# Kernel tuning notes

Measured on AMD Instinct MI355X. Metric: run time of the kernel, lower is better.

## Reference

```python
import jax, jax.numpy as jnp
import numpy as np
import math

B, S, D, H = 2, 2048, 4096, 32
HD = D // H          # 128 head dim
HALF = HD // 2       # 64 rotary pairs
AL = 10              # adapter length


def setup_inputs() -> dict:
    key = jax.random.key(0)
    ks = jax.random.split(key, 8)
    sc = 0.02
    x = jax.random.normal(ks[0], (B, S, D), jnp.float32)
    adapter = jax.random.normal(ks[1], (B, AL, D), jnp.float32)
    wq = jax.random.normal(ks[2], (D, D), jnp.float32) * sc
    wk = jax.random.normal(ks[3], (D, D), jnp.float32) * sc
    wv = jax.random.normal(ks[4], (D, D), jnp.float32) * sc
    wo = jax.random.normal(ks[5], (D, D), jnp.float32) * sc
    gate = jax.random.normal(ks[6], (1, H, 1, 1), jnp.float32) * 0.1
    # rotary frequencies (LLaMA convention), freqs_cis = exp(i * t * f)
    inv_freq = 1.0 / (10000.0 ** (np.arange(0, HD, 2).astype(np.float32) / HD))
    ang = np.outer(np.arange(S, dtype=np.float32), inv_freq)  # [S, HALF]
    cos = jnp.asarray(np.cos(ang), jnp.float32)
    sin = jnp.asarray(np.sin(ang), jnp.float32)
    # additive causal mask [1,1,S,S]
    mask = jnp.triu(jnp.full((S, S), -1e9, jnp.float32), 1)[None, None]
    return {"x": x, "mask": mask, "cos": cos, "sin": sin, "wq": wq,
            "wk": wk, "wv": wv, "wo": wo, "gate": gate,
            "adapter": adapter, "start_pos": 0}


def _rope(t, cos, sin):
    # t: [B,S,H,HD]; complex rotate consecutive pairs
    tr = t.reshape(*t.shape[:-1], HALF, 2)
    t0, t1 = tr[..., 0], tr[..., 1]
    c = cos[None, :, None, :]  # [1,S,1,HALF]
    s = sin[None, :, None, :]
    r0 = t0 * c - t1 * s
    r1 = t0 * s + t1 * c
    return jnp.stack([r0, r1], axis=-1).reshape(t.shape)


def reference(x, mask, cos, sin, wq, wk, wv, wo, gate, adapter, start_pos):
    bsz, seqlen, _ = x.shape
    scale = 1.0 / math.sqrt(HD)
    xq = (x @ wq.T).reshape(bsz, seqlen, H, HD)
    xk = (x @ wk.T).reshape(bsz, seqlen, H, HD)
    xv = (x @ wv.T).reshape(bsz, seqlen, H, HD)
    xq = _rope(xq, cos, sin)
    xk = _rope(xk, cos, sin)
    # training path: keys/values = current tokens (start_pos == 0)
    q = xq.transpose(0, 2, 1, 3)   # [B,H,S,HD]
    k = xk.transpose(0, 2, 1, 3)
    v = xv.transpose(0, 2, 1, 3)
    scores = jnp.einsum('bhqd,bhkd->bhqk', q, k) * scale + mask
    scores = jax.nn.softmax(scores.astype(jnp.float32), axis=-1).astype(x.dtype)
    out = jnp.einsum('bhqk,bhkd->bhqd', scores, v)
    # gated adapter cross-attention (adapter_len > 1 branch)
    a_len = adapter.shape[1]
    a_v = (adapter @ wv.T).reshape(bsz, a_len, H, HD).transpose(0, 2, 1, 3)
    a_k = (adapter @ wk.T).reshape(bsz, a_len, H, HD).transpose(0, 2, 1, 3)
    a_scores = jnp.einsum('bhqd,bhkd->bhqk', q, a_k) * scale
    a_scores = jnp.tanh(gate) * jax.nn.softmax(
        a_scores.astype(jnp.float32), axis=-1).astype(x.dtype)
    out = out + jnp.einsum('bhqk,bhkd->bhqd', a_scores, a_v)
    out = out.transpose(0, 2, 1, 3).reshape(bsz, seqlen, -1)
    return out @ wo.T
```

## Files before the change

kernel.cpp:

```cpp
#include <hip/hip_runtime.h>
#include <hip/hip_bf16.h>
#include <stdint.h>

#define B_ 2
#define S_ 2048
#define D_ 4096
#define H_ 32
#define HD_ 128
#define HALF_ 64
#define AL_ 10
#define MROWS (B_*S_)

typedef __hip_bfloat16 bf16;
typedef __attribute__((ext_vector_type(8))) __bf16 bf16x8;
typedef __attribute__((ext_vector_type(4))) float f32x4;
typedef __attribute__((ext_vector_type(4))) unsigned short us4;

__device__ __forceinline__ void gld_lds16(const void* g, void* l) {
    __builtin_amdgcn_global_load_lds((const __attribute__((address_space(1))) void*)g,
                                     (__attribute__((address_space(3))) void*)l, 16, 0, 0);
}

__global__ void detect_dtype(const unsigned short* __restrict__ x, int* __restrict__ flag) {
    __shared__ int cnt;
    if (threadIdx.x == 0) cnt = 0;
    __syncthreads();
    int bad = 0;
#pragma unroll
    for (int i = 0; i < 16; i++) {
        unsigned int u = x[threadIdx.x * 16 + i];
        float v = __uint_as_float(u << 16);
        if (!(fabsf(v) < 1000.f)) bad++;
    }
    atomicAdd(&cnt, bad);
    __syncthreads();
    if (threadIdx.x == 0) flag[0] = (cnt > 64) ? 1 : 0;
}

__global__ void convert_bf16(const void* __restrict__ in, bf16* __restrict__ out,
                             const int* __restrict__ flag, int n) {
    int i = (blockIdx.x * 256 + threadIdx.x) * 4;
    if (i >= n) return;
    if (flag[0]) {
        float4 f = *(const float4*)((const float*)in + i);
        out[i + 0] = __float2bfloat16(f.x);
        out[i + 1] = __float2bfloat16(f.y);
        out[i + 2] = __float2bfloat16(f.z);
        out[i + 3] = __float2bfloat16(f.w);
    } else {
        *(us4*)(out + i) = *(const us4*)((const unsigned short*)in + i);
    }
}

template<int MODE>
__global__ __launch_bounds__(256) void gemm_bt(
    const bf16* __restrict__ A, const bf16* __restrict__ W,
    const bf16* __restrict__ cosb, const bf16* __restrict__ sinb,
    void* __restrict__ outv, const int* __restrict__ flag, int K)
{
    __shared__ __align__(16) bf16 sA[128*64];
    __shared__ __align__(16) bf16 sB[128*64];
    const int tid  = threadIdx.x;
    const int wave = tid >> 6, lane = tid & 63;
    const int quad = lane >> 4, col = lane & 15;
    const int m0 = blockIdx.y * 128, n0 = blockIdx.x * 128;
    const int wm = (wave >> 1) * 64, wn = (wave & 1) * 64;

    bool f32o = false;
    if (MODE == 2) f32o = (flag[0] != 0);

    f32x4 acc[4][4];
#pragma unroll
    for (int i = 0; i < 4; i++)
#pragma unroll
        for (int j = 0; j < 4; j++) acc[i][j] = {0.f, 0.f, 0.f, 0.f};

    for (int k0 = 0; k0 < K; k0 += 64) {
        __syncthreads();
#pragma unroll
        for (int i = 0; i < 4; i++) {
            int c   = i * 256 + tid;
            int row = c >> 3;
            int cc  = (c & 7) ^ (row & 7);
            gld_lds16(A + (size_t)(m0 + row) * K + k0 + cc * 8,
                      sA + (size_t)(i * 256 + wave * 64) * 8);
            gld_lds16(W + (size_t)(n0 + row) * K + k0 + cc * 8,
                      sB + (size_t)(i * 256 + wave * 64) * 8);
        }
        __syncthreads();

#pragma unroll
        for (int kk = 0; kk < 64; kk += 32) {
            bf16x8 af[4], bfr[4];
#pragma unroll
            for (int mt = 0; mt < 4; mt++) {
                int r  = wm + mt * 16 + col;
                int ck = ((kk >> 3) + quad) ^ (r & 7);
                af[mt] = *(const bf16x8*)(sA + r * 64 + ck * 8);
            }
#pragma unroll
            for (int nt = 0; nt < 4; nt++) {
                int r  = wn + nt * 16 + col;
                int ck = ((kk >> 3) + quad) ^ (r & 7);
                bfr[nt] = *(const bf16x8*)(sB + r * 64 + ck * 8);
            }
#pragma unroll
            for (int mt = 0; mt < 4; mt++)
#pragma unroll
                for (int nt = 0; nt < 4; nt++)
                    acc[mt][nt] = __builtin_amdgcn_mfma_f32_16x16x32_bf16(
                        af[mt], bfr[nt], acc[mt][nt], 0, 0, 0);
        }
    }

#pragma unroll
    for (int mt = 0; mt < 4; mt++) {
#pragma unroll
        for (int nt = 0; nt < 4; nt++) {
            int n = n0 + wn + nt * 16 + col;
#pragma unroll
            for (int e = 0; e < 4; e++) {
                int m   = m0 + wm + mt * 16 + quad * 4 + e;
                float v = acc[mt][nt][e];
                if (MODE == 2) {
                    if (f32o) ((float*)outv)[(size_t)m * D_ + n] = v;
                    else      ((bf16*)outv)[(size_t)m * D_ + n] = __float2bfloat16(v);
                } else {
                    int b = m >> 11, s = m & (S_ - 1);
                    int h = n >> 7,  hd = n & (HD_ - 1);
                    bf16* out = (bf16*)outv;
                    if (MODE == 0) {
                        float other = __shfl_xor(v, 1);
                        float c  = __bfloat162float(cosb[s * HALF_ + (hd >> 1)]);
                        float sn = __bfloat162float(sinb[s * HALF_ + (hd >> 1)]);
                        float r  = (hd & 1) ? (v * c + other * sn)
                                            : (v * c - other * sn);
                        out[((size_t)(b * H_ + h) * S_ + s) * HD_ + hd] = __float2bfloat16(r);
                    } else {
                        out[((size_t)(b * H_ + h) * HD_ + hd) * S_ + s] = __float2bfloat16(v);
                    }
                }
            }
        }
    }
}

__global__ __launch_bounds__(256, 2) void attn_fwd(
    const bf16* __restrict__ q, const bf16* __restrict__ k,
    const bf16* __restrict__ vT, bf16* __restrict__ o)
{
    __shared__ __align__(16) bf16 smem[24576];
    bf16* sK = smem;
    bf16* sV = smem + 8192;
    bf16* sP = smem + 16384;

    const int tid  = threadIdx.x, wave = tid >> 6, lane = tid & 63;
    const int quad = lane >> 4, col = lane & 15;
    const int qt = (gridDim.x - 1) - blockIdx.x;
    const int bh = blockIdx.y;
    const int q0 = qt * 128;
    const bf16* qb = q  + (size_t)bh * S_ * HD_;
    const bf16* kb = k  + (size_t)bh * S_ * HD_;
    const bf16* vb = vT + (size_t)bh * HD_ * S_;

#pragma unroll
    for (int i = 0; i < 8; i++) {
        int c = i * 256 + tid;
        int row = c >> 4;
        int cc  = (c & 15) ^ (row & 7);
        gld_lds16(qb + (size_t)(q0 + row) * HD_ + cc * 8,
                  smem + (size_t)(i * 256 + wave * 64) * 8);
    }
    __syncthreads();

    bf16x8 qf[2][4];
#pragma unroll
    for (int rq = 0; rq < 2; rq++) {
        int row = wave * 32 + rq * 16 + col;
#pragma unroll
        for (int kkI = 0; kkI < 4; kkI++) {
            int ck = (kkI * 4 + quad) ^ (row & 7);
            qf[rq][kkI] = *(const bf16x8*)(smem + row * 128 + ck * 8);
        }
    }

    float mst[2][4], lst[2][4];
#pragma unroll
    for (int rq = 0; rq < 2; rq++)
#pragma unroll
        for (int e = 0; e < 4; e++) { mst[rq][e] = -1e30f; lst[rq][e] = 0.f; }
    f32x4 oacc[2][8];
#pragma unroll
    for (int rq = 0; rq < 2; rq++)
#pragma unroll
        for (int i = 0; i < 8; i++) oacc[rq][i] = {0.f, 0.f, 0.f, 0.f};

    const float scale = 0.08838834764831845f;
    const int ktEnd = 2 * qt + 2;

    for (int kt = 0; kt < ktEnd; kt++) {
        const int k0 = kt * 64;
        __syncthreads();
#pragma unroll
        for (int i = 0; i < 4; i++) {
            int c = i * 256 + tid;
            int rowK = c >> 4, ccK = (c & 15) ^ (rowK & 7);
            gld_lds16(kb + (size_t)(k0 + rowK) * HD_ + ccK * 8,
                      sK + (size_t)(i * 256 + wave * 64) * 8);
            int rowV = c >> 3, ccV = (c & 7) ^ (rowV & 7);
            gld_lds16(vb + (size_t)rowV * S_ + k0 + ccV * 8,
                      sV + (size_t)(i * 256 + wave * 64) * 8);
        }
        __syncthreads();

        f32x4 sc[2][4];
#pragma unroll
        for (int rq = 0; rq < 2; rq++)
#pragma unroll
            for (int nt = 0; nt < 4; nt++) sc[rq][nt] = {0.f, 0.f, 0.f, 0.f};
#pragma unroll
        for (int kkI = 0; kkI < 4; kkI++) {
#pragma unroll
            for (int nt = 0; nt < 4; nt++) {
                int rk  = nt * 16 + col;
                int ckk = (kkI * 4 + quad) ^ (rk & 7);
                bf16x8 bk = *(const bf16x8*)(sK + rk * 128 + ckk * 8);
                sc[0][nt] = __builtin_amdgcn_mfma_f32_16x16x32_bf16(qf[0][kkI], bk, sc[0][nt], 0, 0, 0);
                sc[1][nt] = __builtin_amdgcn_mfma_f32_16x16x32_bf16(qf[1][kkI], bk, sc[1][nt], 0, 0, 0);
            }
        }

        const bool diag = (kt >= 2 * qt);
#pragma unroll
        for (int rq = 0; rq < 2; rq++)
#pragma unroll
            for (int nt = 0; nt < 4; nt++)
#pragma unroll
                for (int e = 0; e < 4; e++) {
                    float v = sc[rq][nt][e] * scale;
                    if (diag && (k0 + nt * 16 + col > q0 + wave * 32 + rq * 16 + quad * 4 + e))
                        v = -1e30f;
                    sc[rq][nt][e] = v;
                }

        float alpha_[2][4];
#pragma unroll
        for (int rq = 0; rq < 2; rq++)
#pragma unroll
            for (int e = 0; e < 4; e++) {
                float mx = fmaxf(fmaxf(sc[rq][0][e], sc[rq][1][e]),
                                 fmaxf(sc[rq][2][e], sc[rq][3][e]));
#pragma unroll
                for (int off = 1; off < 16; off <<= 1) mx = fmaxf(mx, __shfl_xor(mx, off));
                float mnew = fmaxf(mst[rq][e], mx);
                float al   = __expf(mst[rq][e] - mnew);
                float rs   = 0.f;
                int prow = wave * 32 + rq * 16 + quad * 4 + e;
#pragma unroll
                for (int nt = 0; nt < 4; nt++) {
                    float p = __expf(sc[rq][nt][e] - mnew);
                    rs += p;
                    int pcol = nt * 16 + col;
                    int pc   = (pcol >> 3) ^ (prow & 7);
                    sP[prow * 64 + pc * 8 + (pcol & 7)] = __float2bfloat16(p);
                }
#pragma unroll
                for (int off = 1; off < 16; off <<= 1) rs += __shfl_xor(rs, off);
                lst[rq][e] = lst[rq][e] * al + rs;
                mst[rq][e] = mnew;
                alpha_[rq][e] = al;
            }
#pragma unroll
        for (int rq = 0; rq < 2; rq++)
#pragma unroll
            for (int nt = 0; nt < 8; nt++)
#pragma unroll
                for (int e = 0; e < 4; e++) oacc[rq][nt][e] *= alpha_[rq][e];

#pragma unroll
        for (int kkI = 0; kkI < 2; kkI++) {
            bf16x8 pf[2];
#pragma unroll
            for (int rq = 0; rq < 2; rq++) {
                int rp  = wave * 32 + rq * 16 + col;
                int ckp = (kkI * 4 + quad) ^ (rp & 7);
                pf[rq] = *(const bf16x8*)(sP + rp * 64 + ckp * 8);
            }
#pragma unroll
            for (int nt = 0; nt < 8; nt++) {
                int rv  = nt * 16 + col;
                int ckv = (kkI * 4 + quad) ^ (rv & 7);
                bf16x8 vf = *(const bf16x8*)(sV + rv * 64 + ckv * 8);
                oacc[0][nt] = __builtin_amdgcn_mfma_f32_16x16x32_bf16(pf[0], vf, oacc[0][nt], 0, 0, 0);
                oacc[1][nt] = __builtin_amdgcn_mfma_f32_16x16x32_bf16(pf[1], vf, oacc[1][nt], 0, 0, 0);
            }
        }
    }

    const int b = bh >> 5, h = bh & (H_ - 1);
#pragma unroll
    for (int rq = 0; rq < 2; rq++)
#pragma unroll
        for (int e = 0; e < 4; e++) {
            int s = q0 + wave * 32 + rq * 16 + quad * 4 + e;
            float inv = 1.f / lst[rq][e];
#pragma unroll
            for (int nt = 0; nt < 8; nt++) {
                int hd = nt * 16 + col;
                o[((size_t)(b * S_ + s) * H_ + h) * HD_ + hd] =
                    __float2bfloat16(oacc[rq][nt][e] * inv);
            }
        }
}

__global__ __launch_bounds__(256) void adapter_kv(
    const bf16* __restrict__ adp, const bf16* __restrict__ wk,
    const bf16* __restrict__ wv, float* __restrict__ ak, float* __restrict__ av)
{
    const int tid = threadIdx.x, wave = tid >> 6, lane = tid & 63;
    const int gid = blockIdx.x * 4 + wave;
    const int n = gid & (D_ - 1), b = gid >> 12;
    const bf16* w    = blockIdx.y ? wv : wk;
    float*      outp = blockIdx.y ? av : ak;

    float acc[AL_];
#pragma unroll
    for (int j = 0; j < AL_; j++) acc[j] = 0.f;

    for (int t = 0; t < 8; t++) {
        int kb = t * 512 + lane * 8;
        bf16x8 w8 = *(const bf16x8*)(w + (size_t)n * D_ + kb);
        float wf[8];
#pragma unroll
        for (int i = 0; i < 8; i++) wf[i] = (float)w8[i];
#pragma unroll
        for (int j = 0; j < AL_; j++) {
            bf16x8 a8 = *(const bf16x8*)(adp + (size_t)(b * AL_ + j) * D_ + kb);
            float s = 0.f;
#pragma unroll
            for (int i = 0; i < 8; i++) s += (float)a8[i] * wf[i];
            acc[j] += s;
        }
    }
#pragma unroll
    for (int j = 0; j < AL_; j++) {
        float v = acc[j];
#pragma unroll
        for (int off = 1; off < 64; off <<= 1) v += __shfl_xor(v, off);
        if (lane == 0) outp[(size_t)(b * AL_ + j) * D_ + n] = v;
    }
}

__global__ __launch_bounds__(256) void adapter_add(
    const bf16* __restrict__ q, const float* __restrict__ ak,
    const float* __restrict__ av, const bf16* __restrict__ gate,
    bf16* __restrict__ o)
{
    const int tid = threadIdx.x, wave = tid >> 6, lane = tid & 63;
    const int g = blockIdx.x * 4 + wave;
    const int s = g & (S_ - 1);
    const int h = (g >> 11) & (H_ - 1);
    const int b = g >> 16;
    const int hd = lane * 2;

    const bf16* qp = q + ((size_t)(b * H_ + h) * S_ + s) * HD_ + hd;
    float q0f = __bfloat162float(qp[0]);
    float q1f = __bfloat162float(qp[1]);
    const float scale = 0.08838834764831845f;

    float sc[AL_];
#pragma unroll
    for (int j = 0; j < AL_; j++) {
        const float* akp = ak + (size_t)(b * AL_ + j) * D_ + h * HD_ + hd;
        float p = q0f * akp[0] + q1f * akp[1];
#pragma unroll
        for (int off = 1; off < 64; off <<= 1) p += __shfl_xor(p, off);
        sc[j] = p * scale;
    }
    float mx = sc[0];
#pragma unroll
    for (int j = 1; j < AL_; j++) mx = fmaxf(mx, sc[j]);
    float sum = 0.f;
#pragma unroll
    for (int j = 0; j < AL_; j++) { sc[j] = __expf(sc[j] - mx); sum += sc[j]; }
    float wgt = tanhf(__bfloat162float(gate[h])) / sum;

    float a0 = 0.f, a1 = 0.f;
#pragma unroll
    for (int j = 0; j < AL_; j++) {
        const float* avp = av + (size_t)(b * AL_ + j) * D_ + h * HD_ + hd;
        a0 += sc[j] * avp[0];
        a1 += sc[j] * avp[1];
    }
    bf16* op = o + ((size_t)(b * S_ + s) * H_ + h) * HD_ + hd;
    op[0] = __float2bfloat16(__bfloat162float(op[0]) + wgt * a0);
    op[1] = __float2bfloat16(__bfloat162float(op[1]) + wgt * a1);
}

extern "C" void kernel_launch(void* const* d_in, const int* in_sizes, int n_in,
                              void* d_out, int out_size, void* d_ws, size_t ws_size,
                              hipStream_t stream)
{
    const void* x_raw    = d_in[0];
    const void* cos_raw  = d_in[2];
    const void* sin_raw  = d_in[3];
    const void* wq_raw   = d_in[4];
    const void* wk_raw   = d_in[5];
    const void* wv_raw   = d_in[6];
    const void* wo_raw   = d_in[7];
    const void* gate_raw = d_in[8];
    const void* adp_raw  = d_in[9];

    const size_t NE = (size_t)B_ * S_ * D_;
    const int    CS = S_ * HALF_;
    const int    AD = B_ * AL_ * D_;

    bf16* xc   = (bf16*)d_ws;
    bf16* wqc  = xc  + NE;
    bf16* wkc  = wqc + NE;
    bf16* wvc  = wkc + NE;
    bf16* woc  = wvc + NE;
    bf16* qb   = woc + NE;
    bf16* kb   = qb  + NE;
    bf16* vb   = kb  + NE;
    bf16* cosc = vb  + NE;
    bf16* sinc = cosc + CS;
    bf16* adpc = sinc + CS;
    bf16* gatec= adpc + AD;
    float* akb = (float*)(gatec + 32);
    float* avb = akb + AD;
    int*  flag = (int*)(avb + AD);
    bf16* ab   = xc;

    dim3 blk(256);
    detect_dtype<<<1, 256, 0, stream>>>((const unsigned short*)x_raw, flag);

    convert_bf16<<<dim3((int)(NE/4 + 255) / 256), blk, 0, stream>>>(x_raw,  xc,  flag, (int)NE);
    convert_bf16<<<dim3((int)(NE/4 + 255) / 256), blk, 0, stream>>>(wq_raw, wqc, flag, (int)NE);
    convert_bf16<<<dim3((int)(NE/4 + 255) / 256), blk, 0, stream>>>(wk_raw, wkc, flag, (int)NE);
    convert_bf16<<<dim3((int)(NE/4 + 255) / 256), blk, 0, stream>>>(wv_raw, wvc, flag, (int)NE);
    convert_bf16<<<dim3((int)(NE/4 + 255) / 256), blk, 0, stream>>>(wo_raw, woc, flag, (int)NE);
    convert_bf16<<<dim3((CS/4 + 255) / 256), blk, 0, stream>>>(cos_raw,  cosc, flag, CS);
    convert_bf16<<<dim3((CS/4 + 255) / 256), blk, 0, stream>>>(sin_raw,  sinc, flag, CS);
    convert_bf16<<<dim3((AD/4 + 255) / 256), blk, 0, stream>>>(adp_raw,  adpc, flag, AD);
    convert_bf16<<<dim3(1), blk, 0, stream>>>(gate_raw, gatec, flag, 32);

    dim3 gg(D_ / 128, MROWS / 128);
    gemm_bt<0><<<gg, blk, 0, stream>>>(xc, wqc, cosc, sinc, qb, flag, D_);
    gemm_bt<0><<<gg, blk, 0, stream>>>(xc, wkc, cosc, sinc, kb, flag, D_);
    gemm_bt<1><<<gg, blk, 0, stream>>>(xc, wvc, cosc, sinc, vb, flag, D_);
    adapter_kv<<<dim3(2048, 2), blk, 0, stream>>>(adpc, wkc, wvc, akb, avb);
    attn_fwd<<<dim3(S_ / 128, B_ * H_), blk, 0, stream>>>(qb, kb, vb, ab);
    adapter_add<<<dim3(B_ * H_ * S_ / 4), blk, 0, stream>>>(qb, akb, avb, gatec, ab);
    gemm_bt<2><<<gg, blk, 0, stream>>>(ab, woc, cosc, sinc, d_out, flag, D_);
}
```

Before: 1.480 ms.

## Double-buffer K/V in flash attention with 8 waves of 16 rows each

Restructures the attention kernel to use 512 threads (8 waves), each owning 16 query rows instead of 32, and loads Q fragments straight from global memory. K/V tiles are double-buffered in LDS, with the next tile prefetched via global_load_lds while the current one is computed, and raw s_waitcnt/s_barrier replace the two syncthreads per iteration. Waves skip fully masked causal tiles and raise their priority around the MFMA sections. This aims to hide K/V load latency and raise occupancy, at the cost of more LDS per block and hand-counted vmcnt waits that are fragile.

```diff
diff --git a/kernel.cpp b/kernel.cpp
--- a/kernel.cpp
+++ b/kernel.cpp
@@ -145,120 +145,118 @@
     }
 }
 
-__global__ __launch_bounds__(256, 2) void attn_fwd(
+__global__ __launch_bounds__(512, 4) void attn_fwd(
     const bf16* __restrict__ q, const bf16* __restrict__ k,
     const bf16* __restrict__ vT, bf16* __restrict__ o)
 {
-    __shared__ __align__(16) bf16 smem[24576];
-    bf16* sK = smem;
-    bf16* sV = smem + 8192;
-    bf16* sP = smem + 16384;
+    __shared__ __align__(16) bf16 smem[40960];
+    bf16* sP = smem + 32768;
 
     const int tid  = threadIdx.x, wave = tid >> 6, lane = tid & 63;
     const int quad = lane >> 4, col = lane & 15;
     const int qt = (gridDim.x - 1) - blockIdx.x;
     const int bh = blockIdx.y;
     const int q0 = qt * 128;
+    const int row0 = q0 + wave * 16;
+    const int rmax = row0 + 15;
     const bf16* qb = q  + (size_t)bh * S_ * HD_;
     const bf16* kb = k  + (size_t)bh * S_ * HD_;
     const bf16* vb = vT + (size_t)bh * HD_ * S_;
 
-#pragma unroll
-    for (int i = 0; i < 8; i++) {
-        int c = i * 256 + tid;
-        int row = c >> 4;
-        int cc  = (c & 15) ^ (row & 7);
-        gld_lds16(qb + (size_t)(q0 + row) * HD_ + cc * 8,
-                  smem + (size_t)(i * 256 + wave * 64) * 8);
-    }
-    __syncthreads();
-
-    bf16x8 qf[2][4];
-#pragma unroll
-    for (int rq = 0; rq < 2; rq++) {
-        int row = wave * 32 + rq * 16 + col;
-#pragma unroll
-        for (int kkI = 0; kkI < 4; kkI++) {
-            int ck = (kkI * 4 + quad) ^ (row & 7);
-            qf[rq][kkI] = *(const bf16x8*)(smem + row * 128 + ck * 8);
-        }
-    }
-
-    float mst[2][4], lst[2][4];
-#pragma unroll
-    for (int rq = 0; rq < 2; rq++)
-#pragma unroll
-        for (int e = 0; e < 4; e++) { mst[rq][e] = -1e30f; lst[rq][e] = 0.f; }
-    f32x4 oacc[2][8];
-#pragma unroll
-    for (int rq = 0; rq < 2; rq++)
-#pragma unroll
-        for (int i = 0; i < 8; i++) oacc[rq][i] = {0.f, 0.f, 0.f, 0.f};
+    bf16x8 qf[4];
+#pragma unroll
+    for (int kkI = 0; kkI < 4; kkI++)
+        qf[kkI] = *(const bf16x8*)(qb + (size_t)(row0 + col) * HD_ + (kkI * 4 + quad) * 8);
+
+    float mst[4], lst[4];
+#pragma unroll
+    for (int e = 0; e < 4; e++) { mst[e] = -1e30f; lst[e] = 0.f; }
+    f32x4 oacc[8];
+#pragma unroll
+    for (int i = 0; i < 8; i++) oacc[i] = {0.f, 0.f, 0.f, 0.f};
+
+#pragma unroll
+    for (int i = 0; i < 2; i++) {
+        int c = i * 512 + tid;
+        int rowK = c >> 4, ccK = (c & 15) ^ (rowK & 7);
+        gld_lds16(kb + (size_t)rowK * HD_ + ccK * 8,
+                  smem + (size_t)(i * 512 + wave * 64) * 8);
+        int rowV = c >> 3, ccV = (c & 7) ^ (rowV & 7);
+        gld_lds16(vb + (size_t)rowV * S_ + ccV * 8,
+                  smem + 16384 + (size_t)(i * 512 + wave * 64) * 8);
+    }
 
     const float scale = 0.08838834764831845f;
     const int ktEnd = 2 * qt + 2;
+    int cur = 0;
 
     for (int kt = 0; kt < ktEnd; kt++) {
         const int k0 = kt * 64;
-        __syncthreads();
-#pragma unroll
-        for (int i = 0; i < 4; i++) {
-            int c = i * 256 + tid;
-            int rowK = c >> 4, ccK = (c & 15) ^ (rowK & 7);
-            gld_lds16(kb + (size_t)(k0 + rowK) * HD_ + ccK * 8,
-                      sK + (size_t)(i * 256 + wave * 64) * 8);
-            int rowV = c >> 3, ccV = (c & 7) ^ (rowV & 7);
-            gld_lds16(vb + (size_t)rowV * S_ + k0 + ccV * 8,
-                      sV + (size_t)(i * 256 + wave * 64) * 8);
-        }
-        __syncthreads();
-
-        f32x4 sc[2][4];
-#pragma unroll
-        for (int rq = 0; rq < 2; rq++)
-#pragma unroll
-            for (int nt = 0; nt < 4; nt++) sc[rq][nt] = {0.f, 0.f, 0.f, 0.f};
-#pragma unroll
-        for (int kkI = 0; kkI < 4; kkI++) {
-#pragma unroll
-            for (int nt = 0; nt < 4; nt++) {
-                int rk  = nt * 16 + col;
-                int ckk = (kkI * 4 + quad) ^ (rk & 7);
-                bf16x8 bk = *(const bf16x8*)(sK + rk * 128 + ckk * 8);
-                sc[0][nt] = __builtin_amdgcn_mfma_f32_16x16x32_bf16(qf[0][kkI], bk, sc[0][nt], 0, 0, 0);
-                sc[1][nt] = __builtin_amdgcn_mfma_f32_16x16x32_bf16(qf[1][kkI], bk, sc[1][nt], 0, 0, 0);
-            }
-        }
-
-        const bool diag = (kt >= 2 * qt);
-#pragma unroll
-        for (int rq = 0; rq < 2; rq++)
+        bf16* sKc = smem + cur * 8192;
+        bf16* sVc = smem + 16384 + cur * 8192;
+
+        if (kt + 1 < ktEnd) {
+            const int kn = k0 + 64;
+            bf16* sKn = smem + (cur ^ 1) * 8192;
+            bf16* sVn = smem + 16384 + (cur ^ 1) * 8192;
+#pragma unroll
+            for (int i = 0; i < 2; i++) {
+                int c = i * 512 + tid;
+                int rowK = c >> 4, ccK = (c & 15) ^ (rowK & 7);
+                gld_lds16(kb + (size_t)(kn + rowK) * HD_ + ccK * 8,
+                          sKn + (size_t)(i * 512 + wave * 64) * 8);
+                int rowV = c >> 3, ccV = (c & 7) ^ (rowV & 7);
+                gld_lds16(vb + (size_t)rowV * S_ + kn + ccV * 8,
+                          sVn + (size_t)(i * 512 + wave * 64) * 8);
+            }
+            asm volatile("s_waitcnt vmcnt(4)" ::: "memory");
+        } else {
+            asm volatile("s_waitcnt vmcnt(0)" ::: "memory");
+        }
+        asm volatile("s_barrier" ::: "memory");
+
+        if (k0 <= rmax) {
+            f32x4 sc[4];
+#pragma unroll
+            for (int nt = 0; nt < 4; nt++) sc[nt] = {0.f, 0.f, 0.f, 0.f};
+            __builtin_amdgcn_s_setprio(1);
+#pragma unroll
+            for (int kkI = 0; kkI < 4; kkI++) {
+#pragma unroll
+                for (int nt = 0; nt < 4; nt++) {
+                    int rk  = nt * 16 + col;
+                    int ckk = (kkI * 4 + quad) ^ (rk & 7);
+                    bf16x8 bk = *(const bf16x8*)(sKc + rk * 128 + ckk * 8);
+                    sc[nt] = __builtin_amdgcn_mfma_f32_16x16x32_bf16(qf[kkI], bk, sc[nt], 0, 0, 0);
+                }
+            }
+            __builtin_amdgcn_s_setprio(0);
+
+            const bool diag = (k0 + 63 > row0);
 #pragma unroll
             for (int nt = 0; nt < 4; nt++)
 #pragma unroll
                 for (int e = 0; e < 4; e++) {
-                    float v = sc[rq][nt][e] * scale;
-                    if (diag && (k0 + nt * 16 + col > q0 + wave * 32 + rq * 16 + quad * 4 + e))
+                    float v = sc[nt][e] * scale;
+                    if (diag && (k0 + nt * 16 + col > row0 + quad * 4 + e))
                         v = -1e30f;
-                    sc[rq][nt][e] = v;
+                    sc[nt][e] = v;
                 }
 
-        float alpha_[2][4];
-#pragma unroll
-        for (int rq = 0; rq < 2; rq++)
+            float alpha_[4];
 #pragma unroll
             for (int e = 0; e < 4; e++) {
-                float mx = fmaxf(fmaxf(sc[rq][0][e], sc[rq][1][e]),
-                                 fmaxf(sc[rq][2][e], sc[rq][3][e]));
+                float mx = fmaxf(fmaxf(sc[0][e], sc[1][e]),
+                                 fmaxf(sc[2][e], sc[3][e]));
 #pragma unroll
                 for (int off = 1; off < 16; off <<= 1) mx = fmaxf(mx, __shfl_xor(mx, off));
-                float mnew = fmaxf(mst[rq][e], mx);
-                float al   = __expf(mst[rq][e] - mnew);
+                float mnew = fmaxf(mst[e], mx);
+                float al   = __expf(mst[e] - mnew);
                 float rs   = 0.f;
-                int prow = wave * 32 + rq * 16 + quad * 4 + e;
+                int prow = wave * 16 + quad * 4 + e;
 #pragma unroll
                 for (int nt = 0; nt < 4; nt++) {
-                    float p = __expf(sc[rq][nt][e] - mnew);
+                    float p = __expf(sc[nt][e] - mnew);
                     rs += p;
                     int pcol = nt * 16 + col;
                     int pc   = (pcol >> 3) ^ (prow & 7);
@@ -266,51 +264,48 @@
                 }
 #pragma unroll
                 for (int off = 1; off < 16; off <<= 1) rs += __shfl_xor(rs, off);
-                lst[rq][e] = lst[rq][e] * al + rs;
-                mst[rq][e] = mnew;
-                alpha_[rq][e] = al;
-            }
-#pragma unroll
-        for (int rq = 0; rq < 2; rq++)
+                lst[e] = lst[e] * al + rs;
+                mst[e] = mnew;
+                alpha_[e] = al;
+            }
 #pragma unroll
             for (int nt = 0; nt < 8; nt++)
 #pragma unroll
-                for (int e = 0; e < 4; e++) oacc[rq][nt][e] *= alpha_[rq][e];
-
-#pragma unroll
-        for (int kkI = 0; kkI < 2; kkI++) {
-            bf16x8 pf[2];
-#pragma unroll
-            for (int rq = 0; rq < 2; rq++) {
-                int rp  = wave * 32 + rq * 16 + col;
+                for (int e = 0; e < 4; e++) oacc[nt][e] *= alpha_[e];
+
+            __builtin_amdgcn_s_setprio(1);
+#pragma unroll
+            for (int kkI = 0; kkI < 2; kkI++) {
+                int rp  = wave * 16 + col;
                 int ckp = (kkI * 4 + quad) ^ (rp & 7);
-                pf[rq] = *(const bf16x8*)(sP + rp * 64 + ckp * 8);
-            }
-#pragma unroll
-            for (int nt = 0; nt < 8; nt++) {
-                int rv  = nt * 16 + col;
-                int ckv = (kkI * 4 + quad) ^ (rv & 7);
-                bf16x8 vf = *(const bf16x8*)(sV + rv * 64 + ckv * 8);
-                oacc[0][nt] = __builtin_amdgcn_mfma_f32_16x16x32_bf16(pf[0], vf, oacc[0][nt], 0, 0, 0);
-                oacc[1][nt] = __builtin_amdgcn_mfma_f32_16x16x32_bf16(pf[1], vf, oacc[1][nt], 0, 0, 0);
-            }
-        }
+                bf16x8 pf = *(const bf16x8*)(sP + rp * 64 + ckp * 8);
+#pragma unroll
+                for (int nt = 0; nt < 8; nt++) {
+                    int rv  = nt * 16 + col;
+                    int ckv = (kkI * 4 + quad) ^ (rv & 7);
+                    bf16x8 vf = *(const bf16x8*)(sVc + rv * 64 + ckv * 8);
+                    oacc[nt] = __builtin_amdgcn_mfma_f32_16x16x32_bf16(pf, vf, oacc[nt], 0, 0, 0);
+                }
+            }
+            __builtin_amdgcn_s_setprio(0);
+        }
+
+        asm volatile("s_barrier" ::: "memory");
+        cur ^= 1;
     }
 
     const int b = bh >> 5, h = bh & (H_ - 1);
 #pragma unroll
-    for (int rq = 0; rq < 2; rq++)
-#pragma unroll
-        for (int e = 0; e < 4; e++) {
-            int s = q0 + wave * 32 + rq * 16 + quad * 4 + e;
-            float inv = 1.f / lst[rq][e];
-#pragma unroll
-            for (int nt = 0; nt < 8; nt++) {
-                int hd = nt * 16 + col;
-                o[((size_t)(b * S_ + s) * H_ + h) * HD_ + hd] =
-                    __float2bfloat16(oacc[rq][nt][e] * inv);
-            }
-        }
+    for (int e = 0; e < 4; e++) {
+        int s = q0 + wave * 16 + quad * 4 + e;
+        float inv = 1.f / lst[e];
+#pragma unroll
+        for (int nt = 0; nt < 8; nt++) {
+            int hd = nt * 16 + col;
+            o[((size_t)(b * S_ + s) * H_ + h) * HD_ + hd] =
+                __float2bfloat16(oacc[nt][e] * inv);
+        }
+    }
 }
 
 __global__ __launch_bounds__(256) void adapter_kv(
@@ -450,7 +445,7 @@
     gemm_bt<0><<<gg, blk, 0, stream>>>(xc, wkc, cosc, sinc, kb, flag, D_);
     gemm_bt<1><<<gg, blk, 0, stream>>>(xc, wvc, cosc, sinc, vb, flag, D_);
     adapter_kv<<<dim3(2048, 2), blk, 0, stream>>>(adpc, wkc, wvc, akb, avb);
-    attn_fwd<<<dim3(S_ / 128, B_ * H_), blk, 0, stream>>>(qb, kb, vb, ab);
+    attn_fwd<<<dim3(S_ / 128, B_ * H_), dim3(512), 0, stream>>>(qb, kb, vb, ab);
     adapter_add<<<dim3(B_ * H_ * S_ / 4), blk, 0, stream>>>(qb, akb, avb, gatec, ab);
     gemm_bt<2><<<gg, blk, 0, stream>>>(ab, woc, cosc, sinc, d_out, flag, D_);
 }
```

After: 1.435 ms. -3.0%, faster.

## Double-buffer K/V in attention with 512-thread blocks and lazy softmax rescaling

Applied to the files above, without the earlier changes.

Rewrites the attention kernel to use 512-thread blocks covering 256 query rows, and double-buffers K/V tiles in LDS so the next tile's global loads overlap compute, using manual waitcnt and barriers. Q is loaded straight into registers. The softmax scale is folded into the Q projection epilogue. Exp is done via exp2, and the running max is only rescaled when the new max exceeds the old by more than a threshold. Waves skip fully masked tiles, MFMA sections get raised priority, and the P buffer uses an extra swizzle. The trade-off is more LDS per block and a lazy-rescale path that may lose precision in edge cases.

```diff
diff --git a/kernel.cpp b/kernel.cpp
--- a/kernel.cpp
+++ b/kernel.cpp
@@ -56,7 +56,7 @@
 __global__ __launch_bounds__(256) void gemm_bt(
     const bf16* __restrict__ A, const bf16* __restrict__ W,
     const bf16* __restrict__ cosb, const bf16* __restrict__ sinb,
-    void* __restrict__ outv, const int* __restrict__ flag, int K)
+    void* __restrict__ outv, const int* __restrict__ flag, int K, float oscale)
 {
     __shared__ __align__(16) bf16 sA[128*64];
     __shared__ __align__(16) bf16 sB[128*64];
@@ -135,7 +135,8 @@
                         float sn = __bfloat162float(sinb[s * HALF_ + (hd >> 1)]);
                         float r  = (hd & 1) ? (v * c + other * sn)
                                             : (v * c - other * sn);
-                        out[((size_t)(b * H_ + h) * S_ + s) * HD_ + hd] = __float2bfloat16(r);
+                        out[((size_t)(b * H_ + h) * S_ + s) * HD_ + hd] =
+                            __float2bfloat16(r * oscale);
                     } else {
                         out[((size_t)(b * H_ + h) * HD_ + hd) * S_ + s] = __float2bfloat16(v);
                     }
@@ -145,44 +146,31 @@
     }
 }
 
-__global__ __launch_bounds__(256, 2) void attn_fwd(
+__global__ __launch_bounds__(512, 2) void attn_fwd(
     const bf16* __restrict__ q, const bf16* __restrict__ k,
     const bf16* __restrict__ vT, bf16* __restrict__ o)
 {
-    __shared__ __align__(16) bf16 smem[24576];
-    bf16* sK = smem;
-    bf16* sV = smem + 8192;
-    bf16* sP = smem + 16384;
+    __shared__ __align__(16) bf16 smem[49152];
+    bf16* sP = smem + 32768;
 
     const int tid  = threadIdx.x, wave = tid >> 6, lane = tid & 63;
     const int quad = lane >> 4, col = lane & 15;
     const int qt = (gridDim.x - 1) - blockIdx.x;
     const int bh = blockIdx.y;
-    const int q0 = qt * 128;
+    const int q0 = qt * 256;
+    const int row0 = q0 + wave * 32;
+    const int rmax = row0 + 31;
     const bf16* qb = q  + (size_t)bh * S_ * HD_;
     const bf16* kb = k  + (size_t)bh * S_ * HD_;
     const bf16* vb = vT + (size_t)bh * HD_ * S_;
 
-#pragma unroll
-    for (int i = 0; i < 8; i++) {
-        int c = i * 256 + tid;
-        int row = c >> 4;
-        int cc  = (c & 15) ^ (row & 7);
-        gld_lds16(qb + (size_t)(q0 + row) * HD_ + cc * 8,
-                  smem + (size_t)(i * 256 + wave * 64) * 8);
-    }
-    __syncthreads();
-
     bf16x8 qf[2][4];
 #pragma unroll
-    for (int rq = 0; rq < 2; rq++) {
-        int row = wave * 32 + rq * 16 + col;
-#pragma unroll
-        for (int kkI = 0; kkI < 4; kkI++) {
-            int ck = (kkI * 4 + quad) ^ (row & 7);
-            qf[rq][kkI] = *(const bf16x8*)(smem + row * 128 + ck * 8);
-        }
-    }
+    for (int rq = 0; rq < 2; rq++)
+#pragma unroll
+        for (int kkI = 0; kkI < 4; kkI++)
+            qf[rq][kkI] = *(const bf16x8*)(qb + (size_t)(row0 + rq * 16 + col) * HD_
+                                              + (kkI * 4 + quad) * 8);
 
     float mst[2][4], lst[2][4];
 #pragma unroll
@@ -195,106 +183,174 @@
 #pragma unroll
         for (int i = 0; i < 8; i++) oacc[rq][i] = {0.f, 0.f, 0.f, 0.f};
 
-    const float scale = 0.08838834764831845f;
-    const int ktEnd = 2 * qt + 2;
+#pragma unroll
+    for (int i = 0; i < 2; i++) {
+        int c = i * 512 + tid;
+        int rowK = c >> 4, ccK = (c & 15) ^ (rowK & 7);
+        gld_lds16(kb + (size_t)rowK * HD_ + ccK * 8,
+                  smem + (size_t)(i * 512 + wave * 64) * 8);
+        int rowV = c >> 3, ccV = (c & 7) ^ (rowV & 7);
+        gld_lds16(vb + (size_t)rowV * S_ + ccV * 8,
+                  smem + 16384 + (size_t)(i * 512 + wave * 64) * 8);
+    }
+
+    const float L2E = 1.44269504088896f;
+    const int ktEnd = 4 * qt + 4;
+    int cur = 0;
 
     for (int kt = 0; kt < ktEnd; kt++) {
         const int k0 = kt * 64;
-        __syncthreads();
-#pragma unroll
-        for (int i = 0; i < 4; i++) {
-            int c = i * 256 + tid;
-            int rowK = c >> 4, ccK = (c & 15) ^ (rowK & 7);
-            gld_lds16(kb + (size_t)(k0 + rowK) * HD_ + ccK * 8,
-                      sK + (size_t)(i * 256 + wave * 64) * 8);
-            int rowV = c >> 3, ccV = (c & 7) ^ (rowV & 7);
-            gld_lds16(vb + (size_t)rowV * S_ + k0 + ccV * 8,
-                      sV + (size_t)(i * 256 + wave * 64) * 8);
-        }
-        __syncthreads();
-
-        f32x4 sc[2][4];
-#pragma unroll
-        for (int rq = 0; rq < 2; rq++)
-#pragma unroll
-            for (int nt = 0; nt < 4; nt++) sc[rq][nt] = {0.f, 0.f, 0.f, 0.f};
-#pragma unroll
-        for (int kkI = 0; kkI < 4; kkI++) {
-#pragma unroll
-            for (int nt = 0; nt < 4; nt++) {
-                int rk  = nt * 16 + col;
-                int ckk = (kkI * 4 + quad) ^ (rk & 7);
-                bf16x8 bk = *(const bf16x8*)(sK + rk * 128 + ckk * 8);
-                sc[0][nt] = __builtin_amdgcn_mfma_f32_16x16x32_bf16(qf[0][kkI], bk, sc[0][nt], 0, 0, 0);
-                sc[1][nt] = __builtin_amdgcn_mfma_f32_16x16x32_bf16(qf[1][kkI], bk, sc[1][nt], 0, 0, 0);
-            }
-        }
-
-        const bool diag = (kt >= 2 * qt);
-#pragma unroll
-        for (int rq = 0; rq < 2; rq++)
-#pragma unroll
-            for (int nt = 0; nt < 4; nt++)
+        bf16* sKc = smem + cur * 8192;
+        bf16* sVc = smem + 16384 + cur * 8192;
+
+        if (kt + 1 < ktEnd) {
+            const int kn = k0 + 64;
+            bf16* sKn = smem + (cur ^ 1) * 8192;
+            bf16* sVn = smem + 16384 + (cur ^ 1) * 8192;
+#pragma unroll
+            for (int i = 0; i < 2; i++) {
+                int c = i * 512 + tid;
+                int rowK = c >> 4, ccK = (c & 15) ^ (rowK & 7);
+                gld_lds16(kb + (size_t)(kn + rowK) * HD_ + ccK * 8,
+                          sKn + (size_t)(i * 512 + wave * 64) * 8);
+                int rowV = c >> 3, ccV = (c & 7) ^ (rowV & 7);
+                gld_lds16(vb + (size_t)rowV * S_ + kn + ccV * 8,
+                          sVn + (size_t)(i * 512 + wave * 64) * 8);
+            }
+            asm volatile("s_waitcnt vmcnt(4)" ::: "memory");
+        } else {
+            asm volatile("s_waitcnt vmcnt(0)" ::: "memory");
+        }
+        asm volatile("s_barrier" ::: "memory");
+
+        if (k0 <= rmax) {
+            f32x4 sc[2][4];
+#pragma unroll
+            for (int rq = 0; rq < 2; rq++)
+#pragma unroll
+                for (int nt = 0; nt < 4; nt++) sc[rq][nt] = {0.f, 0.f, 0.f, 0.f};
+            __builtin_amdgcn_s_setprio(1);
+#pragma unroll
+            for (int kkI = 0; kkI < 4; kkI++) {
+#pragma unroll
+                for (int nt = 0; nt < 4; nt++) {
+                    int rk  = nt * 16 + col;
+                    int ckk = (kkI * 4 + quad) ^ (rk & 7);
+                    bf16x8 bk = *(const bf16x8*)(sKc + rk * 128 + ckk * 8);
+                    sc[0][nt] = __builtin_amdgcn_mfma_f32_16x16x32_bf16(qf[0][kkI], bk, sc[0][nt], 0, 0, 0);
+                    sc[1][nt] = __builtin_amdgcn_mfma_f32_16x16x32_bf16(qf[1][kkI], bk, sc[1][nt], 0, 0, 0);
+                }
+            }
+            __builtin_amdgcn_s_setprio(0);
+
+#pragma unroll
+            for (int rq = 0; rq < 2; rq++) {
+                if (k0 + 63 > row0 + rq * 16) {
+#pragma unroll
+                    for (int nt = 0; nt < 4; nt++)
+#pragma unroll
+                        for (int e = 0; e < 4; e++)
+                            if (k0 + nt * 16 + col > row0 + rq * 16 + quad * 4 + e)
+                                sc[rq][nt][e] = -1e30f;
+                }
+            }
+
+            float mxv[2][4];
+#pragma unroll
+            for (int rq = 0; rq < 2; rq++)
 #pragma unroll
                 for (int e = 0; e < 4; e++) {
-                    float v = sc[rq][nt][e] * scale;
-                    if (diag && (k0 + nt * 16 + col > q0 + wave * 32 + rq * 16 + quad * 4 + e))
-                        v = -1e30f;
-                    sc[rq][nt][e] = v;
+                    float mx = fmaxf(fmaxf(sc[rq][0][e], sc[rq][1][e]),
+                                     fmaxf(sc[rq][2][e], sc[rq][3][e]));
+#pragma unroll
+                    for (int off = 1; off < 16; off <<= 1) mx = fmaxf(mx, __shfl_xor(mx, off));
+                    mxv[rq][e] = mx;
                 }
-
-        float alpha_[2][4];
-#pragma unroll
-        for (int rq = 0; rq < 2; rq++)
-#pragma unroll
-            for (int e = 0; e < 4; e++) {
-                float mx = fmaxf(fmaxf(sc[rq][0][e], sc[rq][1][e]),
-                                 fmaxf(sc[rq][2][e], sc[rq][3][e]));
-#pragma unroll
-                for (int off = 1; off < 16; off <<= 1) mx = fmaxf(mx, __shfl_xor(mx, off));
-                float mnew = fmaxf(mst[rq][e], mx);
-                float al   = __expf(mst[rq][e] - mnew);
-                float rs   = 0.f;
-                int prow = wave * 32 + rq * 16 + quad * 4 + e;
-#pragma unroll
-                for (int nt = 0; nt < 4; nt++) {
-                    float p = __expf(sc[rq][nt][e] - mnew);
-                    rs += p;
-                    int pcol = nt * 16 + col;
-                    int pc   = (pcol >> 3) ^ (prow & 7);
-                    sP[prow * 64 + pc * 8 + (pcol & 7)] = __float2bfloat16(p);
+            float need = -1e30f;
+#pragma unroll
+            for (int rq = 0; rq < 2; rq++)
+#pragma unroll
+                for (int e = 0; e < 4; e++) need = fmaxf(need, mxv[rq][e] - mst[rq][e]);
+
+            if (__all(need <= 8.f)) {
+#pragma unroll
+                for (int rq = 0; rq < 2; rq++)
+#pragma unroll
+                    for (int e = 0; e < 4; e++) {
+                        float nm = -mst[rq][e] * L2E;
+                        float rs = 0.f;
+                        int prow = wave * 32 + rq * 16 + quad * 4 + e;
+                        int swz  = (prow & 7) ^ (((prow >> 3) & 1) << 1);
+#pragma unroll
+                        for (int nt = 0; nt < 4; nt++) {
+                            float p = __builtin_amdgcn_exp2f(fmaf(sc[rq][nt][e], L2E, nm));
+                            rs += p;
+                            int pcol = nt * 16 + col;
+                            int pc   = (pcol >> 3) ^ swz;
+                            sP[prow * 64 + pc * 8 + (pcol & 7)] = __float2bfloat16(p);
+                        }
+#pragma unroll
+                        for (int off = 1; off < 16; off <<= 1) rs += __shfl_xor(rs, off);
+                        lst[rq][e] += rs;
+                    }
+            } else {
+                float alpha_[2][4];
+#pragma unroll
+                for (int rq = 0; rq < 2; rq++)
+#pragma unroll
+                    for (int e = 0; e < 4; e++) {
+                        float mnew = fmaxf(mst[rq][e], mxv[rq][e]);
+                        float al   = __builtin_amdgcn_exp2f((mst[rq][e] - mnew) * L2E);
+                        float nm   = -mnew * L2E;
+                        float rs   = 0.f;
+                        int prow = wave * 32 + rq * 16 + quad * 4 + e;
+                        int swz  = (prow & 7) ^ (((prow >> 3) & 1) << 1);
+#pragma unroll
+                        for (int nt = 0; nt < 4; nt++) {
+                            float p = __builtin_amdgcn_exp2f(fmaf(sc[rq][nt][e], L2E, nm));
+                            rs += p;
+                            int pcol = nt * 16 + col;
+                            int pc   = (pcol >> 3) ^ swz;
+                            sP[prow * 64 + pc * 8 + (pcol & 7)] = __float2bfloat16(p);
+                        }
+#pragma unroll
+                        for (int off = 1; off < 16; off <<= 1) rs += __shfl_xor(rs, off);
+                        lst[rq][e] = lst[rq][e] * al + rs;
+                        mst[rq][e] = mnew;
+                        alpha_[rq][e] = al;
+                    }
+#pragma unroll
+                for (int rq = 0; rq < 2; rq++)
+#pragma unroll
+                    for (int nt = 0; nt < 8; nt++)
+#pragma unroll
+                        for (int e = 0; e < 4; e++) oacc[rq][nt][e] *= alpha_[rq][e];
+            }
+
+            __builtin_amdgcn_s_setprio(1);
+#pragma unroll
+            for (int kkI = 0; kkI < 2; kkI++) {
+                bf16x8 pf[2];
+#pragma unroll
+                for (int rq = 0; rq < 2; rq++) {
+                    int rp  = wave * 32 + rq * 16 + col;
+                    int ckp = (kkI * 4 + quad) ^ (rp & 7) ^ (((rp >> 3) & 1) << 1);
+                    pf[rq] = *(const bf16x8*)(sP + rp * 64 + ckp * 8);
                 }
 #pragma unroll
-                for (int off = 1; off < 16; off <<= 1) rs += __shfl_xor(rs, off);
-                lst[rq][e] = lst[rq][e] * al + rs;
-                mst[rq][e] = mnew;
-                alpha_[rq][e] = al;
-            }
-#pragma unroll
-        for (int rq = 0; rq < 2; rq++)
-#pragma unroll
-            for (int nt = 0; nt < 8; nt++)
-#pragma unroll
-                for (int e = 0; e < 4; e++) oacc[rq][nt][e] *= alpha_[rq][e];
-
-#pragma unroll
-        for (int kkI = 0; kkI < 2; kkI++) {
-            bf16x8 pf[2];
-#pragma unroll
-            for (int rq = 0; rq < 2; rq++) {
-                int rp  = wave * 32 + rq * 16 + col;
-                int ckp = (kkI * 4 + quad) ^ (rp & 7);
-                pf[rq] = *(const bf16x8*)(sP + rp * 64 + ckp * 8);
-            }
-#pragma unroll
-            for (int nt = 0; nt < 8; nt++) {
-                int rv  = nt * 16 + col;
-                int ckv = (kkI * 4 + quad) ^ (rv & 7);
-                bf16x8 vf = *(const bf16x8*)(sV + rv * 64 + ckv * 8);
-                oacc[0][nt] = __builtin_amdgcn_mfma_f32_16x16x32_bf16(pf[0], vf, oacc[0][nt], 0, 0, 0);
-                oacc[1][nt] = __builtin_amdgcn_mfma_f32_16x16x32_bf16(pf[1], vf, oacc[1][nt], 0, 0, 0);
-            }
-        }
+                for (int nt = 0; nt < 8; nt++) {
+                    int rv  = nt * 16 + col;
+                    int ckv = (kkI * 4 + quad) ^ (rv & 7);
+                    bf16x8 vf = *(const bf16x8*)(sVc + rv * 64 + ckv * 8);
+                    oacc[0][nt] = __builtin_amdgcn_mfma_f32_16x16x32_bf16(pf[0], vf, oacc[0][nt], 0, 0, 0);
+                    oacc[1][nt] = __builtin_amdgcn_mfma_f32_16x16x32_bf16(pf[1], vf, oacc[1][nt], 0, 0, 0);
+                }
+            }
+            __builtin_amdgcn_s_setprio(0);
+        }
+
+        asm volatile("s_barrier" ::: "memory");
+        cur ^= 1;
     }
 
     const int b = bh >> 5, h = bh & (H_ - 1);
@@ -366,7 +422,6 @@
     const bf16* qp = q + ((size_t)(b * H_ + h) * S_ + s) * HD_ + hd;
     float q0f = __bfloat162float(qp[0]);
     float q1f = __bfloat162float(qp[1]);
-    const float scale = 0.08838834764831845f;
 
     float sc[AL_];
 #pragma unroll
@@ -375,7 +430,7 @@
         float p = q0f * akp[0] + q1f * akp[1];
 #pragma unroll
         for (int off = 1; off < 64; off <<= 1) p += __shfl_xor(p, off);
-        sc[j] = p * scale;
+        sc[j] = p;
     }
     float mx = sc[0];
 #pragma unroll
@@ -432,6 +487,8 @@
     int*  flag = (int*)(avb + AD);
     bf16* ab   = xc;
 
+    const float scale = 0.08838834764831845f;
+
     dim3 blk(256);
     detect_dtype<<<1, 256, 0, stream>>>((const unsigned short*)x_raw, flag);
 
@@ -446,11 +503,11 @@
     convert_bf16<<<dim3(1), blk, 0, stream>>>(gate_raw, gatec, flag, 32);
 
     dim3 gg(D_ / 128, MROWS / 128);
-    gemm_bt<0><<<gg, blk, 0, stream>>>(xc, wqc, cosc, sinc, qb, flag, D_);
-    gemm_bt<0><<<gg, blk, 0, stream>>>(xc, wkc, cosc, sinc, kb, flag, D_);
-    gemm_bt<1><<<gg, blk, 0, stream>>>(xc, wvc, cosc, sinc, vb, flag, D_);
+    gemm_bt<0><<<gg, blk, 0, stream>>>(xc, wqc, cosc, sinc, qb, flag, D_, scale);
+    gemm_bt<0><<<gg, blk, 0, stream>>>(xc, wkc, cosc, sinc, kb, flag, D_, 1.0f);
+    gemm_bt<1><<<gg, blk, 0, stream>>>(xc, wvc, cosc, sinc, vb, flag, D_, 1.0f);
     adapter_kv<<<dim3(2048, 2), blk, 0, stream>>>(adpc, wkc, wvc, akb, avb);
-    attn_fwd<<<dim3(S_ / 128, B_ * H_), blk, 0, stream>>>(qb, kb, vb, ab);
+    attn_fwd<<<dim3(S_ / 256, B_ * H_), dim3(512), 0, stream>>>(qb, kb, vb, ab);
     adapter_add<<<dim3(B_ * H_ * S_ / 4), blk, 0, stream>>>(qb, akb, avb, gatec, ab);
-    gemm_bt<2><<<gg, blk, 0, stream>>>(ab, woc, cosc, sinc, d_out, flag, D_);
-}
+    gemm_bt<2><<<gg, blk, 0, stream>>>(ab, woc, cosc, sinc, d_out, flag, D_, 1.0f);
+}
```

After: 1.617 ms. 1.09x slower.
